# Optimization experiments

Measured on AMD Instinct MI355X. Metric: run time of the kernel, lower is better.

## Reference

```python
import jax, jax.numpy as jnp
import numpy as np

IN_SIZE = 256    # network input size
N_NODES = 1024   # hidden+output nodes, processed in topological order
DEG = 32         # fixed fan-in per node
BATCH = 16384
OUT_SIZE = 16    # last OUT_SIZE nodes are output nodes (is_output=True)


def setup_inputs() -> dict:
    key = jax.random.key(0)
    kx, kw = jax.random.split(key)
    x = jax.random.normal(kx, (BATCH, IN_SIZE), dtype=jnp.float32)
    weights = jax.random.normal(kw, (N_NODES, DEG), dtype=jnp.float32)
    # node i may only read network inputs and outputs of nodes < i
    rng = np.random.default_rng(0)
    in_idxs = np.stack([rng.integers(0, IN_SIZE + i, size=DEG) for i in range(N_NODES)])
    return {"x": x, "weights": weights, "in_idxs": jnp.asarray(in_idxs, dtype=jnp.int32)}


def reference(x, weights, in_idxs):
    B = x.shape[0]
    # activs buffer: [B, in_size + n_nodes + 1], inputs written to front
    activs = jnp.zeros((B, IN_SIZE + N_NODES + 1), dtype=x.dtype)
    activs = activs.at[:, :IN_SIZE].set(x)
    write_pos = IN_SIZE + jnp.arange(N_NODES, dtype=jnp.int32)

    def step(a, node):
        idxs, w, pos = node
        gathered = jnp.take(a, idxs, axis=1)      # [B, DEG]  index_select
        n_out = jnp.tanh(gathered @ w)            # [B]       matmul + activation
        a = a.at[:, pos].set(n_out)               # sequential write into buffer
        return a, n_out

    _, outs = jax.lax.scan(step, activs, (in_idxs, weights, write_pos))
    # output nodes are the last OUT_SIZE nodes; torch.tensor(out) stacks -> [OUT_SIZE, B]
    return outs[-OUT_SIZE:]
```

## Files before the change

kernel.cpp:

```cpp
#include <hip/hip_runtime.h>

#define IN_SIZE 256
#define N_NODES 1024
#define DEG 32
#define BATCH 16384
#define OUT_SIZE 16
#define COLS 4
#define N_ROWS (IN_SIZE + N_NODES)
#define NPAIR (N_NODES / 2)

__device__ __forceinline__ unsigned short f2bf_rne(float f) {
    const unsigned u = __float_as_uint(f);
    return (unsigned short)((u + 0x7FFFu + ((u >> 16) & 1u)) >> 16);
}

__device__ __forceinline__ float tanh6(float z) {
    const float s = __expf(-2.0f * fabsf(z));
    const float r = __builtin_amdgcn_rcpf(1.0f + s);
    return copysignf(fmaf(-s, r, r), z);
}

template <int CTRL>
__device__ __forceinline__ float dpp_add(float v) {
    return v + __int_as_float(__builtin_amdgcn_mov_dpp(__float_as_int(v), CTRL, 0xF, 0xF, true));
}
__device__ __forceinline__ float dpp_ror8(float v) {
    return __int_as_float(__builtin_amdgcn_mov_dpp(__float_as_int(v), 0x128, 0xF, 0xF, true));
}

__global__ __launch_bounds__(64) void ne_detect(const void* __restrict__ xraw,
                                                int* __restrict__ flag) {
    const unsigned short* xb = (const unsigned short*)xraw;
    const int tid = threadIdx.x;
    int plausible = 0;
    for (int k = tid; k < 2048; k += 64) {
        const float v = __uint_as_float((unsigned)xb[2 * k] << 16);
        const float a = fabsf(v);
        plausible += (a == 0.0f) || (a > 1e-3f && a < 1e3f) ? 1 : 0;
    }
    for (int off = 32; off > 0; off >>= 1) plausible += __shfl_down(plausible, off);
    if (tid == 0) *flag = (plausible >= (2048 * 9) / 10) ? 1 : 0;
}

__global__ __launch_bounds__(256) void ne_prep(const void* __restrict__ wraw,
                                               const int* __restrict__ idxs,
                                               int4* __restrict__ pki,
                                               float4* __restrict__ pkw,
                                               float4* __restrict__ hzr,
                                               const int* __restrict__ flag) {
    const int isbf16 = *flag;
    const int tid = blockIdx.x * 256 + threadIdx.x;
    const int stride = gridDim.x * 256;
    const unsigned short* wb = (const unsigned short*)wraw;
    const float* wsrc = (const float*)wraw;
    for (int k = tid; k < N_NODES * 8; k += stride) {
        const int n = k >> 3, qq = k & 7;
        const int e = n * DEG + qq * 4;
        pki[k] = make_int4(idxs[e], idxs[e + 1], idxs[e + 2], idxs[e + 3]);
        float w0 = isbf16 ? __uint_as_float((unsigned)wb[e + 0] << 16) : wsrc[e + 0];
        float w1 = isbf16 ? __uint_as_float((unsigned)wb[e + 1] << 16) : wsrc[e + 1];
        float w2 = isbf16 ? __uint_as_float((unsigned)wb[e + 2] << 16) : wsrc[e + 2];
        float w3 = isbf16 ? __uint_as_float((unsigned)wb[e + 3] << 16) : wsrc[e + 3];
        pkw[k] = make_float4(w0, w1, w2, w3);
    }
    for (int n = tid; n < N_NODES; n += stride) {
        float h1 = 0.0f, h2 = 0.0f, h3 = 0.0f;
        const int r1 = IN_SIZE + n - 1, r2 = IN_SIZE + n - 2, r3 = IN_SIZE + n - 3;
        for (int r = 0; r < DEG; ++r) {
            const int id = idxs[n * DEG + r];
            const float w = isbf16 ? __uint_as_float((unsigned)wb[n * DEG + r] << 16)
                                   : wsrc[n * DEG + r];
            if (n >= 1 && id == r1) h1 += w;
            if (n >= 2 && id == r2) h2 += w;
            if (n >= 3 && id == r3) h3 += w;
        }
        const float4 hp = (n & 1) ? make_float4(h2, h3, h1, 0.0f)
                                  : make_float4(h1, h2, 0.0f, 0.0f);
#pragma unroll
        for (int r = 0; r < 8; ++r) hzr[n * 8 + r] = hp;
    }
}

__global__ __launch_bounds__(64) void ne_forward(const void* __restrict__ xraw,
                                                 const int4* __restrict__ pki,
                                                 const float4* __restrict__ pkw,
                                                 const float4* __restrict__ hzr,
                                                 void* __restrict__ outraw,
                                                 const int* __restrict__ flag) {
    __shared__ float act[N_ROWS * COLS];
    const int lane = threadIdx.x;
    const int q = lane & 7;
    const int h = (lane >> 3) & 1;
    const int c = lane >> 4;
    const int l15 = lane & 15;
    const int c0 = blockIdx.x * COLS;
    const int isbf16 = *flag;
    float* outf = (float*)outraw;
    unsigned short* outb = (unsigned short*)outraw;

    {
        float4* az = (float4*)(act + IN_SIZE * COLS);
#pragma unroll
        for (int t = 0; t < 16; ++t) az[t * 64 + lane] = make_float4(0.f, 0.f, 0.f, 0.f);
    }
    {
        const int b = c;
        if (isbf16) {
            const unsigned short* xb =
                (const unsigned short*)xraw + (size_t)(c0 + b) * IN_SIZE + l15 * 16;
#pragma unroll
            for (int t = 0; t < 2; ++t) {
                const uint4 v = *(const uint4*)(xb + t * 8);
                const int k0 = l15 * 16 + t * 8;
                act[(k0 + 0) * COLS + b] = __uint_as_float(v.x << 16);
                act[(k0 + 1) * COLS + b] = __uint_as_float(v.x & 0xFFFF0000u);
                act[(k0 + 2) * COLS + b] = __uint_as_float(v.y << 16);
                act[(k0 + 3) * COLS + b] = __uint_as_float(v.y & 0xFFFF0000u);
                act[(k0 + 4) * COLS + b] = __uint_as_float(v.z << 16);
                act[(k0 + 5) * COLS + b] = __uint_as_float(v.z & 0xFFFF0000u);
                act[(k0 + 6) * COLS + b] = __uint_as_float(v.w << 16);
                act[(k0 + 7) * COLS + b] = __uint_as_float(v.w & 0xFFFF0000u);
            }
        } else {
            const float* xs = (const float*)xraw + (size_t)(c0 + b) * IN_SIZE + l15 * 16;
#pragma unroll
            for (int t = 0; t < 4; ++t) {
                const float4 v = *(const float4*)(xs + t * 4);
                const int k0 = l15 * 16 + t * 4;
                act[(k0 + 0) * COLS + b] = v.x;
                act[(k0 + 1) * COLS + b] = v.y;
                act[(k0 + 2) * COLS + b] = v.z;
                act[(k0 + 3) * COLS + b] = v.w;
            }
        }
    }

    const int4 i0 = pki[0 * 16 + l15];
    const int4 i1 = pki[1 * 16 + l15];
    float gA0 = act[i0.x * COLS + c], gA1 = act[i0.y * COLS + c],
          gA2 = act[i0.z * COLS + c], gA3 = act[i0.w * COLS + c];
    float gB0 = act[i1.x * COLS + c], gB1 = act[i1.y * COLS + c],
          gB2 = act[i1.z * COLS + c], gB3 = act[i1.w * COLS + c];
    int4   idv0 = pki[2 * 16 + l15], idv1 = pki[3 * 16 + l15];
    float4 wv0 = pkw[0 * 16 + l15], wv1 = pkw[1 * 16 + l15];
    float4 hz0 = hzr[0 * 16 + l15], hz1 = hzr[1 * 16 + l15];
    float tpA = 0.0f, tpB = 0.0f;
    const bool hodd = (h == 1);

#define PAIRSTEP(P, G0, G1, G2, G3, IDV, WV, HZ, OUT, CLAMP)                           \
    {                                                                                  \
        float z = G0 * WV.x; z = fmaf(G1, WV.y, z);                                    \
        z = fmaf(G2, WV.z, z); z = fmaf(G3, WV.w, z);                                  \
        z = dpp_add<0xB1>(z); z = dpp_add<0x4E>(z); z = dpp_add<0x141>(z);             \
        z = fmaf(HZ.x, tpB, z); z = fmaf(HZ.y, tpA, z);                                \
        const float t1 = tanh6(z);                                                     \
        const float to = dpp_ror8(t1);                   \
        z = fmaf(HZ.z, to, z);                                                         \
        const float t = tanh6(z);                  \
        if (q == 0) {                                                                  \
            act[(IN_SIZE + 2 * (P) + h) * COLS + c] = t;                               \
            if (OUT) {                                                                 \
                const size_t o =                                                       \
                    (size_t)(2 * (P) + h - (N_NODES - OUT_SIZE)) * BATCH + c0 + c;     \
                if (isbf16) outb[o] = f2bf_rne(t); else outf[o] = t;                   \
            }                                                                          \
        }                                                                              \
        const float o2 = dpp_ror8(t);                        \
        tpA = hodd ? o2 : t;                                  \
        tpB = hodd ? t : o2;                                  \
               \
        G0 = act[IDV.x * COLS + c]; G1 = act[IDV.y * COLS + c];                        \
        G2 = act[IDV.z * COLS + c]; G3 = act[IDV.w * COLS + c];                        \
                \
        { const int Pn = (CLAMP) ? (((P) + 4 < NPAIR) ? (P) + 4 : NPAIR - 1) : (P) + 4;\
          const int Pw = (CLAMP) ? (((P) + 2 < NPAIR) ? (P) + 2 : NPAIR - 1) : (P) + 2;\
          IDV = pki[(Pn << 4) + l15];                                                  \
          WV  = pkw[(Pw << 4) + l15];                                                  \
          HZ  = hzr[(Pw << 4) + l15]; }                                                \
    }

#pragma unroll 1
    for (int P = 0; P < NPAIR - 8; P += 2) {
        PAIRSTEP(P,     gA0, gA1, gA2, gA3, idv0, wv0, hz0, 0, 0)
        PAIRSTEP(P + 1, gB0, gB1, gB2, gB3, idv1, wv1, hz1, 0, 0)
    }
    {
        const int P = NPAIR - 8;
        PAIRSTEP(P + 0, gA0, gA1, gA2, gA3, idv0, wv0, hz0, 1, 1)
        PAIRSTEP(P + 1, gB0, gB1, gB2, gB3, idv1, wv1, hz1, 1, 1)
        PAIRSTEP(P + 2, gA0, gA1, gA2, gA3, idv0, wv0, hz0, 1, 1)
        PAIRSTEP(P + 3, gB0, gB1, gB2, gB3, idv1, wv1, hz1, 1, 1)
        PAIRSTEP(P + 4, gA0, gA1, gA2, gA3, idv0, wv0, hz0, 1, 1)
        PAIRSTEP(P + 5, gB0, gB1, gB2, gB3, idv1, wv1, hz1, 1, 1)
        PAIRSTEP(P + 6, gA0, gA1, gA2, gA3, idv0, wv0, hz0, 1, 1)
        PAIRSTEP(P + 7, gB0, gB1, gB2, gB3, idv1, wv1, hz1, 1, 1)
    }
#undef PAIRSTEP
}

extern "C" void kernel_launch(void* const* d_in, const int* in_sizes, int n_in,
                              void* d_out, int out_size, void* d_ws, size_t ws_size,
                              hipStream_t stream) {
    const void* x   = d_in[0];
    const void* w   = d_in[1];
    const int* idxs = (const int*)d_in[2];

    int4*   pki = (int4*)d_ws;
    float4* pkw = (float4*)((char*)d_ws + (size_t)256 * 1024);
    float4* hzr = (float4*)((char*)d_ws + (size_t)512 * 1024);
    int* flag   = (int*)((char*)d_ws + ((ws_size - 16) & ~(size_t)15));

    ne_detect<<<1, 64, 0, stream>>>(x, flag);
    ne_prep<<<32, 256, 0, stream>>>(w, idxs, pki, pkw, hzr, flag);

    ne_forward<<<dim3(BATCH / COLS), dim3(64), 0, stream>>>(x, pki, pkw, hzr, d_out, flag);
}
```

Measured before the change: 289.1 us.

## Pipeline gather-dot one pair ahead and patch up to five recent dependencies

The gather and dot-product for the next node pair now run before the current pair's tanh chain, so the LDS gather latency overlaps the serial activation work. Because the look-ahead dot product reads stale values for the last five node outputs, the prep kernel precomputes correction weights for distances 1 to 5. Those corrections are applied with FMAs on the two previous pairs' outputs plus an intra-pair term. This lengthens the dependency-correction chain and adds registers in exchange for hiding gather latency on the critical path.

Measured after the change: 291.4 us. Within noise of the previous version (+0.8%).

```diff
diff --git a/kernel.cpp b/kernel.cpp
--- a/kernel.cpp
+++ b/kernel.cpp
@@ -46,7 +46,8 @@
                                                const int* __restrict__ idxs,
                                                int4* __restrict__ pki,
                                                float4* __restrict__ pkw,
-                                               float4* __restrict__ hzr,
+                                               float4* __restrict__ hza,
+                                               float* __restrict__ hcc,
                                                const int* __restrict__ flag) {
     const int isbf16 = *flag;
     const int tid = blockIdx.x * 256 + threadIdx.x;
@@ -64,27 +65,30 @@
         pkw[k] = make_float4(w0, w1, w2, w3);
     }
     for (int n = tid; n < N_NODES; n += stride) {
-        float h1 = 0.0f, h2 = 0.0f, h3 = 0.0f;
-        const int r1 = IN_SIZE + n - 1, r2 = IN_SIZE + n - 2, r3 = IN_SIZE + n - 3;
+        float h1 = 0.f, h2 = 0.f, h3 = 0.f, h4 = 0.f, h5 = 0.f;
         for (int r = 0; r < DEG; ++r) {
             const int id = idxs[n * DEG + r];
+            if (id < IN_SIZE) continue;
+            const int d = IN_SIZE + n - id;
+            if (d < 1 || d > 5) continue;
             const float w = isbf16 ? __uint_as_float((unsigned)wb[n * DEG + r] << 16)
                                    : wsrc[n * DEG + r];
-            if (n >= 1 && id == r1) h1 += w;
-            if (n >= 2 && id == r2) h2 += w;
-            if (n >= 3 && id == r3) h3 += w;
+            if (d == 1) h1 += w; else if (d == 2) h2 += w; else if (d == 3) h3 += w;
+            else if (d == 4) h4 += w; else h5 += w;
         }
-        const float4 hp = (n & 1) ? make_float4(h2, h3, h1, 0.0f)
-                                  : make_float4(h1, h2, 0.0f, 0.0f);
-#pragma unroll
-        for (int r = 0; r < 8; ++r) hzr[n * 8 + r] = hp;
+        const float4 a = (n & 1) ? make_float4(h2, h3, h4, h5)
+                                 : make_float4(h2, h1, h4, h3);
+        const float hc = (n & 1) ? h1 : 0.0f;
+#pragma unroll
+        for (int r = 0; r < 8; ++r) { hza[n * 8 + r] = a; hcc[n * 8 + r] = hc; }
     }
 }
 
 __global__ __launch_bounds__(64) void ne_forward(const void* __restrict__ xraw,
                                                  const int4* __restrict__ pki,
                                                  const float4* __restrict__ pkw,
-                                                 const float4* __restrict__ hzr,
+                                                 const float4* __restrict__ hza,
+                                                 const float* __restrict__ hcc,
                                                  void* __restrict__ outraw,
                                                  const int* __restrict__ flag) {
     __shared__ float act[N_ROWS * COLS];
@@ -135,65 +139,92 @@
         }
     }
 
-    const int4 i0 = pki[0 * 16 + l15];
-    const int4 i1 = pki[1 * 16 + l15];
-    float gA0 = act[i0.x * COLS + c], gA1 = act[i0.y * COLS + c],
-          gA2 = act[i0.z * COLS + c], gA3 = act[i0.w * COLS + c];
-    float gB0 = act[i1.x * COLS + c], gB1 = act[i1.y * COLS + c],
-          gB2 = act[i1.z * COLS + c], gB3 = act[i1.w * COLS + c];
-    int4   idv0 = pki[2 * 16 + l15], idv1 = pki[3 * 16 + l15];
-    float4 wv0 = pkw[0 * 16 + l15], wv1 = pkw[1 * 16 + l15];
-    float4 hz0 = hzr[0 * 16 + l15], hz1 = hzr[1 * 16 + l15];
-    float tpA = 0.0f, tpB = 0.0f;
-    const bool hodd = (h == 1);
-
-#define PAIRSTEP(P, G0, G1, G2, G3, IDV, WV, HZ, OUT, CLAMP)                           \
+    float accA, accB;
+    float gA0, gA1, gA2, gA3, gB0, gB1, gB2, gB3;
+    {
+        const int4 it = pki[(0 << 4) + l15];
+        const float4 wt = pkw[(0 << 4) + l15];
+        const float x0 = act[it.x * COLS + c], x1 = act[it.y * COLS + c];
+        const float x2 = act[it.z * COLS + c], x3 = act[it.w * COLS + c];
+        float zr = x0 * wt.x; zr = fmaf(x1, wt.y, zr);
+        zr = fmaf(x2, wt.z, zr); zr = fmaf(x3, wt.w, zr);
+        zr = dpp_add<0xB1>(zr); zr = dpp_add<0x4E>(zr); zr = dpp_add<0x141>(zr);
+        accA = zr;
+    }
+    {
+        const int4 it = pki[(1 << 4) + l15];
+        gA0 = act[it.x * COLS + c]; gA1 = act[it.y * COLS + c];
+        gA2 = act[it.z * COLS + c]; gA3 = act[it.w * COLS + c];
+    }
+    int4   idv0 = pki[(2 << 4) + l15], idv1 = pki[(3 << 4) + l15];
+    float4 wv0  = pkw[(1 << 4) + l15], wv1  = pkw[(2 << 4) + l15];
+    float4 hza0 = hza[(0 << 4) + l15], hza1 = hza[(1 << 4) + l15];
+    float  hcc0 = hcc[(0 << 4) + l15], hcc1 = hcc[(1 << 4) + l15];
+    float tsP1 = 0.f, toP1 = 0.f, tsP2 = 0.f, toP2 = 0.f;
+
+#define PAIRSTEP(S, GC0, GC1, GC2, GC3, GN0, GN1, GN2, GN3,                            \
+                 IDV, WVV, HZA, HCC, ACCc, ACCn, OUT, CLAMP)                           \
     {                                                                                  \
-        float z = G0 * WV.x; z = fmaf(G1, WV.y, z);                                    \
-        z = fmaf(G2, WV.z, z); z = fmaf(G3, WV.w, z);                                  \
-        z = dpp_add<0xB1>(z); z = dpp_add<0x4E>(z); z = dpp_add<0x141>(z);             \
-        z = fmaf(HZ.x, tpB, z); z = fmaf(HZ.y, tpA, z);                                \
+                                      \
+        float zr = GC0 * WVV.x; zr = fmaf(GC1, WVV.y, zr);                             \
+        zr = fmaf(GC2, WVV.z, zr); zr = fmaf(GC3, WVV.w, zr);                          \
+        zr = dpp_add<0xB1>(zr); zr = dpp_add<0x4E>(zr); zr = dpp_add<0x141>(zr);       \
+        ACCn = zr;                                                                     \
+                \
+        GN0 = act[IDV.x * COLS + c]; GN1 = act[IDV.y * COLS + c];                      \
+        GN2 = act[IDV.z * COLS + c]; GN3 = act[IDV.w * COLS + c];                      \
+                                                               \
+        float z = fmaf(HZA.x, tsP1, ACCc);                                             \
+        z = fmaf(HZA.y, toP1, z);                                                      \
+        z = fmaf(HZA.z, tsP2, z);                                                      \
+        z = fmaf(HZA.w, toP2, z);                                                      \
         const float t1 = tanh6(z);                                                     \
-        const float to = dpp_ror8(t1);                   \
-        z = fmaf(HZ.z, to, z);                                                         \
-        const float t = tanh6(z);                  \
+        z = fmaf(HCC, dpp_ror8(t1), z);                  \
+        const float t = tanh6(z);                                                      \
         if (q == 0) {                                                                  \
-            act[(IN_SIZE + 2 * (P) + h) * COLS + c] = t;                               \
+            act[(IN_SIZE + 2 * (S) + h) * COLS + c] = t;                               \
             if (OUT) {                                                                 \
                 const size_t o =                                                       \
-                    (size_t)(2 * (P) + h - (N_NODES - OUT_SIZE)) * BATCH + c0 + c;     \
+                    (size_t)(2 * (S) + h - (N_NODES - OUT_SIZE)) * BATCH + c0 + c;     \
                 if (isbf16) outb[o] = f2bf_rne(t); else outf[o] = t;                   \
             }                                                                          \
         }                                                                              \
-        const float o2 = dpp_ror8(t);                        \
-        tpA = hodd ? o2 : t;                                  \
-        tpB = hodd ? t : o2;                                  \
-               \
-        G0 = act[IDV.x * COLS + c]; G1 = act[IDV.y * COLS + c];                        \
-        G2 = act[IDV.z * COLS + c]; G3 = act[IDV.w * COLS + c];                        \
-                \
-        { const int Pn = (CLAMP) ? (((P) + 4 < NPAIR) ? (P) + 4 : NPAIR - 1) : (P) + 4;\
-          const int Pw = (CLAMP) ? (((P) + 2 < NPAIR) ? (P) + 2 : NPAIR - 1) : (P) + 2;\
+        tsP2 = tsP1; toP2 = toP1; tsP1 = t; toP1 = dpp_ror8(t);                        \
+                      \
+        { const int Pw = (CLAMP) ? (((S) + 3 < NPAIR) ? (S) + 3 : NPAIR - 1) : (S) + 3;\
+          const int Pn = (CLAMP) ? (((S) + 4 < NPAIR) ? (S) + 4 : NPAIR - 1) : (S) + 4;\
+          const int Ph = (CLAMP) ? (((S) + 2 < NPAIR) ? (S) + 2 : NPAIR - 1) : (S) + 2;\
+          WVV = pkw[(Pw << 4) + l15];                                                  \
           IDV = pki[(Pn << 4) + l15];                                                  \
-          WV  = pkw[(Pw << 4) + l15];                                                  \
-          HZ  = hzr[(Pw << 4) + l15]; }                                                \
+          HZA = hza[(Ph << 4) + l15];                                                  \
+          HCC = hcc[(Ph << 4) + l15]; }                                                \
     }
 
 #pragma unroll 1
-    for (int P = 0; P < NPAIR - 8; P += 2) {
-        PAIRSTEP(P,     gA0, gA1, gA2, gA3, idv0, wv0, hz0, 0, 0)
-        PAIRSTEP(P + 1, gB0, gB1, gB2, gB3, idv1, wv1, hz1, 0, 0)
-    }
-    {
-        const int P = NPAIR - 8;
-        PAIRSTEP(P + 0, gA0, gA1, gA2, gA3, idv0, wv0, hz0, 1, 1)
-        PAIRSTEP(P + 1, gB0, gB1, gB2, gB3, idv1, wv1, hz1, 1, 1)
-        PAIRSTEP(P + 2, gA0, gA1, gA2, gA3, idv0, wv0, hz0, 1, 1)
-        PAIRSTEP(P + 3, gB0, gB1, gB2, gB3, idv1, wv1, hz1, 1, 1)
-        PAIRSTEP(P + 4, gA0, gA1, gA2, gA3, idv0, wv0, hz0, 1, 1)
-        PAIRSTEP(P + 5, gB0, gB1, gB2, gB3, idv1, wv1, hz1, 1, 1)
-        PAIRSTEP(P + 6, gA0, gA1, gA2, gA3, idv0, wv0, hz0, 1, 1)
-        PAIRSTEP(P + 7, gB0, gB1, gB2, gB3, idv1, wv1, hz1, 1, 1)
+    for (int S = 0; S < NPAIR - 8; S += 2) {
+        PAIRSTEP(S,     gA0, gA1, gA2, gA3, gB0, gB1, gB2, gB3,
+                 idv0, wv0, hza0, hcc0, accA, accB, 0, 0)
+        PAIRSTEP(S + 1, gB0, gB1, gB2, gB3, gA0, gA1, gA2, gA3,
+                 idv1, wv1, hza1, hcc1, accB, accA, 0, 0)
+    }
+    {
+        const int S = NPAIR - 8;
+        PAIRSTEP(S + 0, gA0, gA1, gA2, gA3, gB0, gB1, gB2, gB3,
+                 idv0, wv0, hza0, hcc0, accA, accB, 1, 1)
+        PAIRSTEP(S + 1, gB0, gB1, gB2, gB3, gA0, gA1, gA2, gA3,
+                 idv1, wv1, hza1, hcc1, accB, accA, 1, 1)
+        PAIRSTEP(S + 2, gA0, gA1, gA2, gA3, gB0, gB1, gB2, gB3,
+                 idv0, wv0, hza0, hcc0, accA, accB, 1, 1)
+        PAIRSTEP(S + 3, gB0, gB1, gB2, gB3, gA0, gA1, gA2, gA3,
+                 idv1, wv1, hza1, hcc1, accB, accA, 1, 1)
+        PAIRSTEP(S + 4, gA0, gA1, gA2, gA3, gB0, gB1, gB2, gB3,
+                 idv0, wv0, hza0, hcc0, accA, accB, 1, 1)
+        PAIRSTEP(S + 5, gB0, gB1, gB2, gB3, gA0, gA1, gA2, gA3,
+                 idv1, wv1, hza1, hcc1, accB, accA, 1, 1)
+        PAIRSTEP(S + 6, gA0, gA1, gA2, gA3, gB0, gB1, gB2, gB3,
+                 idv0, wv0, hza0, hcc0, accA, accB, 1, 1)
+        PAIRSTEP(S + 7, gB0, gB1, gB2, gB3, gA0, gA1, gA2, gA3,
+                 idv1, wv1, hza1, hcc1, accB, accA, 1, 1)
     }
 #undef PAIRSTEP
 }
@@ -206,12 +237,14 @@
     const int* idxs = (const int*)d_in[2];
 
     int4*   pki = (int4*)d_ws;
-    float4* pkw = (float4*)((char*)d_ws + (size_t)256 * 1024);
-    float4* hzr = (float4*)((char*)d_ws + (size_t)512 * 1024);
+    float4* pkw = (float4*)((char*)d_ws + (size_t)128 * 1024);
+    float4* hza = (float4*)((char*)d_ws + (size_t)256 * 1024);
+    float*  hcc = (float*)((char*)d_ws + (size_t)384 * 1024);
     int* flag   = (int*)((char*)d_ws + ((ws_size - 16) & ~(size_t)15));
 
     ne_detect<<<1, 64, 0, stream>>>(x, flag);
-    ne_prep<<<32, 256, 0, stream>>>(w, idxs, pki, pkw, hzr, flag);
-
-    ne_forward<<<dim3(BATCH / COLS), dim3(64), 0, stream>>>(x, pki, pkw, hzr, d_out, flag);
-}
+    ne_prep<<<32, 256, 0, stream>>>(w, idxs, pki, pkw, hza, hcc, flag);
+
+    ne_forward<<<dim3(BATCH / COLS), dim3(64), 0, stream>>>(x, pki, pkw, hza, hcc,
+                                                            d_out, flag);
+}
```
